# Performance work log

Hardware: AMD Instinct MI355X
Metric: run time of the kernel (lower is better)

## Reference

```python
import jax, jax.numpy as jnp
import numpy as np

SEQ_LEN, BSIZE, DIM_OBJ_QST = 128, 1024, 37
QST_DIM, HIDDEN, SLOTS = 11, 256, 20


def _linear_params(key, out_dim, in_dim):
    kw, kb = jax.random.split(key)
    # xavier_normal for weight, default uniform-ish small bias
    std = (2.0 / (in_dim + out_dim)) ** 0.5
    w = jax.random.normal(kw, (out_dim, in_dim), jnp.float32) * std
    b = jax.random.uniform(kb, (out_dim,), jnp.float32, -0.01, 0.01)
    return w, b


def setup_inputs() -> dict:
    key = jax.random.key(0)
    ks = jax.random.split(key, 10)
    memory_inputs = jax.random.normal(ks[0], (SEQ_LEN, BSIZE, DIM_OBJ_QST), jnp.float32)
    question_inputs = jax.random.normal(ks[1], (BSIZE, QST_DIM), jnp.float32)
    C_w, C_b = _linear_params(ks[2], HIDDEN, DIM_OBJ_QST)
    Q_w, Q_b = _linear_params(ks[3], HIDDEN, QST_DIM)
    H_w, H_b = _linear_params(ks[4], HIDDEN, 2 * HIDDEN)
    U_w, U_b = _linear_params(ks[5], HIDDEN, HIDDEN)
    V_w, V_b = _linear_params(ks[6], HIDDEN, HIDDEN)
    W_w, W_b = _linear_params(ks[7], HIDDEN, HIDDEN)
    J_w, J_b = _linear_params(ks[8], HIDDEN, 3 * HIDDEN)
    prelu_a = jnp.float32(1.0)  # nn.PReLU(init=1), single shared slope
    # nn.Embedding(num_mem_slots, hidden, padding_idx=0), uniform(-sqrt3, sqrt3), row 0 zeroed
    embed = jax.random.uniform(ks[9], (SLOTS, HIDDEN), jnp.float32, -(3.0 ** 0.5), 3.0 ** 0.5)
    embed = embed.at[0].set(0.0)
    return dict(memory_inputs=memory_inputs, question_inputs=question_inputs,
                C_w=C_w, C_b=C_b, Q_w=Q_w, Q_b=Q_b, H_w=H_w, H_b=H_b,
                U_w=U_w, U_b=U_b, V_w=V_w, V_b=V_b, W_w=W_w, W_b=W_b,
                J_w=J_w, J_b=J_b, prelu_a=prelu_a, embed=embed)


def reference(memory_inputs, question_inputs, C_w, C_b, Q_w, Q_b, H_w, H_b,
              U_w, U_b, V_w, V_b, W_w, W_b, J_w, J_b, prelu_a, embed):
    S, B, _ = memory_inputs.shape
    D, M = embed.shape[1], embed.shape[0]

    mi = jax.nn.relu(jnp.einsum('sbi,di->sbd', memory_inputs, C_w) + C_b)  # (S,B,D)
    q = jax.nn.relu(question_inputs @ Q_w.T + Q_b)                          # (B,D)

    # keys: embedding(arange(M)) tiled per batch, flattened to (B*M, D)
    keys = jnp.tile(embed[None, :, :], (B, 1, 1)).reshape(B * M, D)

    def step(memories, sentence):  # sentence: (B,D)
        sent = jnp.repeat(sentence, M, axis=0)                              # (B*M, D)
        gate = jax.nn.sigmoid(jnp.sum(sent * (memories + keys), axis=-1, keepdims=True))
        join = jnp.concatenate([memories @ U_w.T + U_b,
                                sent @ V_w.T + V_b,
                                keys @ W_w.T + W_b], axis=1)                # (B*M, 3D)
        j = jax.nn.relu(join) @ J_w.T + J_b
        cand = jnp.where(j > 0, j, prelu_a * j)                             # PReLU
        upd = memories + gate * cand
        upd = upd / (jnp.linalg.norm(upd, axis=-1, keepdims=True) + 1e-12)
        return upd, None

    memories, _ = jax.lax.scan(step, keys, mi)
    ng = memories.reshape(B, M, D)
    energies = jnp.sum(ng * q[:, None, :], axis=-1)                         # (B,M)
    attn = jax.nn.softmax(energies, axis=-1)
    attended = jnp.sum(ng * attn[:, :, None], axis=1)                       # (B,D)
    out = jax.nn.relu(jnp.concatenate([q, attended], axis=1) @ H_w.T + H_b)
    return out
```

## Files before the change

kernel.cpp:

```cpp
#include <hip/hip_runtime.h>
#include <hip/hip_bf16.h>


#define S_LEN 128
#define BSZ   1024
#define DOBJ  37
#define QD    11

typedef float f32x4 __attribute__((ext_vector_type(4)));
typedef short bf16x8 __attribute__((ext_vector_type(8)));
typedef short bf16x4 __attribute__((ext_vector_type(4)));

#define MFMA16(a, b, c) __builtin_amdgcn_mfma_f32_16x16x32_bf16((a), (b), (c), 0, 0, 0)

__device__ __forceinline__ float b2f(short h) {
    union { unsigned u; float f; } c; c.u = ((unsigned)(unsigned short)h) << 16; return c.f;
}
__device__ __forceinline__ short f2b(float x) {
    union { float f; unsigned u; } c; c.f = x;
    return (short)((c.u + 0x7FFFu + ((c.u >> 16) & 1u)) >> 16);
}
__device__ __forceinline__ unsigned pkbf(float a, float b) {
    union { __hip_bfloat162 h2; unsigned u; } c;
    c.h2 = __float22bfloat162_rn(make_float2(a, b));
    return c.u;
}
__device__ __forceinline__ float ld1(const void* p, int i, bool f32) {
    return f32 ? ((const float*)p)[i] : b2f(((const short*)p)[i]);
}
__device__ __forceinline__ bf16x8 ld8(const void* p, int i, bool f32) {
    if (!f32) return *(const bf16x8*)((const short*)p + i);
    const float* q = (const float*)p + i;
    bf16x8 r;
    #pragma unroll
    for (int e = 0; e < 8; ++e) r[e] = f2b(q[e]);
    return r;
}

__global__ __launch_bounds__(256, 2) void renet_phase1(
    const void* __restrict__ MI, const void* __restrict__ Cw, const void* __restrict__ Cb,
    const void* __restrict__ Vw, const void* __restrict__ Vb, const void* __restrict__ Jw,
    const void* __restrict__ PA, short* __restrict__ mi_out, short* __restrict__ jv_out)
{
    const bool F32 = (*(const unsigned*)PA == 0x3F800000u);
    __shared__ __align__(16) short A[64 * 264];
    __shared__ __align__(16) float MIL[64 * 40];
    __shared__ float VBL[256];

    const int t = threadIdx.x, r0 = blockIdx.x * 64;
    const int wv = t >> 6, lane = t & 63, lr = lane & 15, quad = lane >> 4;

    VBL[t] = ld1(Vb, t, F32);
    for (int c = 0; c < 10; ++c) {
        int idx = c * 256 + t;
        if (idx < 64 * 37) { int i = idx / 37, k = idx - i * 37; MIL[i * 40 + k] = ld1(MI, (r0 + i) * 37 + k, F32); }
    }
    __syncthreads();

    {
        float cw[DOBJ];
        #pragma unroll
        for (int k = 0; k < DOBJ; ++k) cw[k] = ld1(Cw, t * DOBJ + k, F32);
        float cb = ld1(Cb, t, F32);
        for (int i = 0; i < 64; ++i) {
            float a = cb;
            #pragma unroll
            for (int k = 0; k < DOBJ; ++k) a += MIL[i * 40 + k] * cw[k];
            short h = f2b(fmaxf(a, 0.f));
            A[i * 264 + t] = h;
            mi_out[(r0 + i) * 256 + t] = h;
        }
    }
    __syncthreads();

    const f32x4 Z4 = {0.f, 0.f, 0.f, 0.f};
    f32x4 acc[4][4];

    #pragma unroll
    for (int rt = 0; rt < 4; ++rt)
        #pragma unroll
        for (int nt = 0; nt < 4; ++nt) acc[rt][nt] = Z4;
    #pragma unroll
    for (int kt = 0; kt < 8; ++kt) {
        bf16x8 a[4];
        #pragma unroll
        for (int rt = 0; rt < 4; ++rt)
            a[rt] = *(const bf16x8*)&A[(rt * 16 + lr) * 264 + kt * 32 + quad * 8];
        #pragma unroll
        for (int nt = 0; nt < 4; ++nt) {
            int n = wv * 64 + nt * 16 + lr;
            bf16x8 b = ld8(Vw, n * 256 + kt * 32 + quad * 8, F32);
            #pragma unroll
            for (int rt = 0; rt < 4; ++rt) acc[rt][nt] = MFMA16(a[rt], b, acc[rt][nt]);
        }
    }
    __syncthreads();
    #pragma unroll
    for (int nt = 0; nt < 4; ++nt) {
        int n = wv * 64 + nt * 16 + lr;
        float vb = VBL[n];
        #pragma unroll
        for (int rt = 0; rt < 4; ++rt)
            #pragma unroll
            for (int r = 0; r < 4; ++r)
                A[(rt * 16 + quad * 4 + r) * 264 + n] = f2b(fmaxf(acc[rt][nt][r] + vb, 0.f));
    }
    __syncthreads();

    #pragma unroll
    for (int rt = 0; rt < 4; ++rt)
        #pragma unroll
        for (int nt = 0; nt < 4; ++nt) acc[rt][nt] = Z4;
    #pragma unroll
    for (int kt = 0; kt < 8; ++kt) {
        bf16x8 a[4];
        #pragma unroll
        for (int rt = 0; rt < 4; ++rt)
            a[rt] = *(const bf16x8*)&A[(rt * 16 + lr) * 264 + kt * 32 + quad * 8];
        #pragma unroll
        for (int nt = 0; nt < 4; ++nt) {
            int n = wv * 64 + nt * 16 + lr;
            bf16x8 b = ld8(Jw, n * 768 + 256 + kt * 32 + quad * 8, F32);
            #pragma unroll
            for (int rt = 0; rt < 4; ++rt) acc[rt][nt] = MFMA16(a[rt], b, acc[rt][nt]);
        }
    }
    __syncthreads();
    #pragma unroll
    for (int nt = 0; nt < 4; ++nt) {
        int n = wv * 64 + nt * 16 + lr;
        #pragma unroll
        for (int rt = 0; rt < 4; ++rt)
            #pragma unroll
            for (int r = 0; r < 4; ++r)
                A[(rt * 16 + quad * 4 + r) * 264 + n] = f2b(acc[rt][nt][r]);
    }
    __syncthreads();
    for (int c = 0; c < 16; ++c) {
        int idx = c * 1024 + t * 4;
        int i = idx >> 8, k = idx & 255;
        *(ushort4*)&jv_out[(r0 + i) * 256 + k] = *(const ushort4*)&A[i * 264 + k];
    }
}

__global__ __launch_bounds__(512, 2) void renet_recur(
    const short* __restrict__ mi, const short* __restrict__ jv,
    const void* __restrict__ Qin, const void* __restrict__ Qw, const void* __restrict__ Qb,
    const void* __restrict__ Uw, const void* __restrict__ Ub,
    const void* __restrict__ Jw, const void* __restrict__ Jb,
    const void* __restrict__ Ww, const void* __restrict__ Wb,
    const void* __restrict__ Hw, const void* __restrict__ Hb,
    const void* __restrict__ PA, const void* __restrict__ Emb, void* __restrict__ Out)
{
    const bool F32 = (*(const unsigned*)PA == 0x3F800000u);
    __shared__ __align__(16) short LDS[32208];
    short* const A1  = LDS;
    short* const STG = LDS + 15840;
    short* const SJ  = LDS + 26400;
    short* const JWL = LDS + 26928;

    const int t = threadIdx.x;
    const int w8 = t >> 6;
    const int lane = t & 63, lr = lane & 15, quad = lane >> 4;
    const int colb = w8 * 32;
    const float pa = ld1(PA, 0, F32);
    const f32x4 Z4 = {0.f, 0.f, 0.f, 0.f};
    const int bq0 = blockIdx.x * 2;

    float ub2[2][4];
    #pragma unroll
    for (int ct = 0; ct < 2; ++ct)
        #pragma unroll
        for (int r = 0; r < 4; ++r) ub2[ct][r] = ld1(Ub, colb + ct * 16 + quad * 4 + r, F32);

    bf16x8 uf[8][2], jf[8][2];
    #pragma unroll
    for (int kt = 0; kt < 8; ++kt)
        #pragma unroll
        for (int ct = 0; ct < 2; ++ct) {
            uf[kt][ct] = ld8(Uw, (colb + ct * 16 + lr) * 256 + kt * 32 + quad * 8, F32);
            jf[kt][ct] = ld8(Jw, (colb + ct * 16 + lr) * 768 + kt * 32 + quad * 8, F32);
        }

    for (int c = 0; c < 11; ++c) {
        int idx = c * 512 + t;
        if (idx < 20 * 264) {
            int row = idx / 264, k = idx - row * 264;
            A1[(40 + row) * 264 + k] = (k < 256) ? f2b(ld1(Emb, row * 256 + k, F32)) : (short)0;
        }
    }
    __syncthreads();

    {
        const int col = t & 255, grp = t >> 8, m0p = grp * 10;
        float* WKS = (float*)STG;
        float wacc[10];
        #pragma unroll
        for (int mm = 0; mm < 10; ++mm) wacc[mm] = 0.f;
        for (int c = 0; c < 32; ++c) {
            bf16x8 wv8 = ld8(Ww, col * 256 + c * 8, F32);
            float wf[8];
            #pragma unroll
            for (int e = 0; e < 8; ++e) wf[e] = b2f(wv8[e]);
            #pragma unroll
            for (int mm = 0; mm < 10; ++mm) {
                bf16x8 e8 = *(const bf16x8*)&A1[(40 + m0p + mm) * 264 + c * 8];
                float s = 0.f;
                #pragma unroll
                for (int e = 0; e < 8; ++e) s += b2f(e8[e]) * wf[e];
                wacc[mm] += s;
            }
        }
        float wb = ld1(Wb, col, F32);
        #pragma unroll
        for (int mm = 0; mm < 10; ++mm) WKS[(m0p + mm) * 256 + col] = fmaxf(wacc[mm] + wb, 0.f);
    }
    for (int c = 0; c < 21; ++c) {
        int idx = c * 512 + t;
        if (idx < 40 * 264) {
            int row = idx / 264, k = idx - row * 264;
            short v = (k < 256) ? A1[(40 + row % 20) * 264 + k] : (short)0;
            if (k == 256 || k == 257) v = (k == 257) ? (short)0x3F80 : (short)0;
            A1[idx] = v;
        }
    }
    __syncthreads();

    {
        const int col = t & 255, grp = t >> 8, m0p = grp * 10;
        const float* WKS = (const float*)STG;
        const float jb = ld1(Jb, col, F32);
        float jacc[10];
        #pragma unroll
        for (int mm = 0; mm < 10; ++mm) jacc[mm] = 0.f;
        for (int c = 0; c < 32; ++c) {
            bf16x8 j8 = ld8(Jw, col * 768 + 512 + c * 8, F32);
            float jfv[8];
            #pragma unroll
            for (int e = 0; e < 8; ++e) jfv[e] = b2f(j8[e]);
            #pragma unroll
            for (int mm = 0; mm < 10; ++mm) {
                float4 w0 = *(const float4*)&WKS[(m0p + mm) * 256 + c * 8];
                float4 w1 = *(const float4*)&WKS[(m0p + mm) * 256 + c * 8 + 4];
                jacc[mm] += w0.x * jfv[0] + w0.y * jfv[1] + w0.z * jfv[2] + w0.w * jfv[3]
                          + w1.x * jfv[4] + w1.y * jfv[5] + w1.z * jfv[6] + w1.w * jfv[7];
            }
        }
        #pragma unroll
        for (int mm = 0; mm < 10; ++mm) JWL[(m0p + mm) * 264 + col] = f2b(jacc[mm] + jb);
    }

    ushort4 pf_mi = {0, 0, 0, 0};
    if (t < 128) {
        pf_mi = *(const ushort4*)&mi[(bq0 + (t >> 6)) * 256 + (t & 63) * 4];
        *(ushort4*)&SJ[(t >> 6) * 264 + (t & 63) * 4] = pf_mi;
    }
    __syncthreads();

    for (int s = 0; s < S_LEN; ++s) {
        const int parO = (s & 1) << 1, parN = 2 - parO;

        if (s + 1 < S_LEN && t < 128)
            pf_mi = *(const ushort4*)&mi[((s + 1) * BSZ + bq0 + (t >> 6)) * 256 + (t & 63) * 4];

        float sc_o[3];
        #pragma unroll
        for (int nt = 0; nt < 3; ++nt) {
            const int row = ((nt == 0) ? 0 : (nt == 1) ? 16 : 24) + lr;
            sc_o[nt] = 1.f / (sqrtf(*(const float*)&A1[row * 264 + 256 + parO]) + 1e-12f);
        }

        if (w8 < 4) {
            const int base = (w8 == 3) ? 44 : w8 * 16;
            f32x4 ag = Z4;
            #pragma unroll
            for (int kt = 0; kt < 8; ++kt) {
                bf16x8 a = *(const bf16x8*)&SJ[lr * 264 + kt * 32 + quad * 8];
                bf16x8 b = *(const bf16x8*)&A1[(base + lr) * 264 + kt * 32 + quad * 8];
                ag = MFMA16(a, b, ag);
            }
            if (quad == 0) {
                const int row = base + lr;
                float sg = 1.f;
                if (row < 40) sg = 1.f / (sqrtf(*(const float*)&A1[row * 264 + 256 + parO]) + 1e-12f);
                float* gl = (float*)&A1[row * 264 + 260];
                gl[0] = ag[0] * sg; gl[1] = ag[1] * sg;
            }
        }

        f32x4 acc[3][2];
        #pragma unroll
        for (int nt = 0; nt < 3; ++nt) { acc[nt][0] = Z4; acc[nt][1] = Z4; }
        #pragma unroll
        for (int kt = 0; kt < 8; ++kt) {
            bf16x8 b0 = *(const bf16x8*)&A1[(0 + lr) * 264 + kt * 32 + quad * 8];
            bf16x8 b1 = *(const bf16x8*)&A1[(16 + lr) * 264 + kt * 32 + quad * 8];
            bf16x8 b2 = *(const bf16x8*)&A1[(24 + lr) * 264 + kt * 32 + quad * 8];
            acc[0][0] = MFMA16(uf[kt][0], b0, acc[0][0]);
            acc[1][0] = MFMA16(uf[kt][0], b1, acc[1][0]);
            acc[2][0] = MFMA16(uf[kt][0], b2, acc[2][0]);
            acc[0][1] = MFMA16(uf[kt][1], b0, acc[0][1]);
            acc[1][1] = MFMA16(uf[kt][1], b1, acc[1][1]);
            acc[2][1] = MFMA16(uf[kt][1], b2, acc[2][1]);
        }
        #pragma unroll
        for (int nt = 0; nt < 3; ++nt) {
            const int base = (nt == 0) ? 0 : (nt == 1) ? 16 : 24;
            #pragma unroll
            for (int ct = 0; ct < 2; ++ct) {
                uint2 pk;
                pk.x = pkbf(fmaxf(acc[nt][ct][0] * sc_o[nt] + ub2[ct][0], 0.f),
                            fmaxf(acc[nt][ct][1] * sc_o[nt] + ub2[ct][1], 0.f));
                pk.y = pkbf(fmaxf(acc[nt][ct][2] * sc_o[nt] + ub2[ct][2], 0.f),
                            fmaxf(acc[nt][ct][3] * sc_o[nt] + ub2[ct][3], 0.f));
                *(uint2*)&STG[(base + lr) * 264 + colb + ct * 16 + quad * 4] = pk;
            }
        }
        if (t < 40) *(float*)&A1[t * 264 + 256 + parN] = 0.f;
        __syncthreads();

        bf16x4 jv0[2], jv1[2];
        #pragma unroll
        for (int ct = 0; ct < 2; ++ct) {
            jv0[ct] = *(const bf16x4*)&jv[(s * BSZ + bq0) * 256 + colb + ct * 16 + quad * 4];
            jv1[ct] = *(const bf16x4*)&jv[(s * BSZ + bq0 + 1) * 256 + colb + ct * 16 + quad * 4];
        }

        f32x4 acc2[3][2];
        #pragma unroll
        for (int nt = 0; nt < 3; ++nt) { acc2[nt][0] = Z4; acc2[nt][1] = Z4; }
        #pragma unroll
        for (int kt = 0; kt < 8; ++kt) {
            bf16x8 b0 = *(const bf16x8*)&STG[(0 + lr) * 264 + kt * 32 + quad * 8];
            bf16x8 b1 = *(const bf16x8*)&STG[(16 + lr) * 264 + kt * 32 + quad * 8];
            bf16x8 b2 = *(const bf16x8*)&STG[(24 + lr) * 264 + kt * 32 + quad * 8];
            acc2[0][0] = MFMA16(jf[kt][0], b0, acc2[0][0]);
            acc2[1][0] = MFMA16(jf[kt][0], b1, acc2[1][0]);
            acc2[2][0] = MFMA16(jf[kt][0], b2, acc2[2][0]);
            acc2[0][1] = MFMA16(jf[kt][1], b0, acc2[0][1]);
            acc2[1][1] = MFMA16(jf[kt][1], b1, acc2[1][1]);
            acc2[2][1] = MFMA16(jf[kt][1], b2, acc2[2][1]);
        }

        float gate_[3];
        bf16x4 old_[3][2], jw_[3][2];
        #pragma unroll
        for (int nt = 0; nt < 3; ++nt) {
            const int base = (nt == 0) ? 0 : (nt == 1) ? 16 : 24;
            const int row = base + lr;
            const int bi = (row >= 20) ? 1 : 0;
            const int slot = row - bi * 20;
            float gp = ((const float*)&A1[row * 264 + 260])[bi]
                     + ((const float*)&A1[(40 + slot) * 264 + 260])[bi];
            gate_[nt] = 1.f / (1.f + __expf(-gp));
            jw_[nt][0]  = *(const bf16x4*)&JWL[slot * 264 + colb + quad * 4];
            jw_[nt][1]  = *(const bf16x4*)&JWL[slot * 264 + colb + 16 + quad * 4];
            old_[nt][0] = *(const bf16x4*)&A1[row * 264 + colb + quad * 4];
            old_[nt][1] = *(const bf16x4*)&A1[row * 264 + colb + 16 + quad * 4];
        }
        #pragma unroll
        for (int nt = 0; nt < 3; ++nt) {
            const int base = (nt == 0) ? 0 : (nt == 1) ? 16 : 24;
            const int row = base + lr;
            const int bi = (row >= 20) ? 1 : 0;
            float ss = 0.f;
            #pragma unroll
            for (int ct = 0; ct < 2; ++ct) {
                bf16x4 jv4 = bi ? jv1[ct] : jv0[ct];
                float u4[4];
                #pragma unroll
                for (int r = 0; r < 4; ++r) {
                    float j = acc2[nt][ct][r] + b2f(jv4[r]) + b2f(jw_[nt][ct][r]);
                    float cand = j > 0.f ? j : pa * j;
                    float u = b2f(old_[nt][ct][r]) * sc_o[nt] + gate_[nt] * cand;
                    u4[r] = u;
                    ss += u * u;
                }
                uint2 pk;
                pk.x = pkbf(u4[0], u4[1]);
                pk.y = pkbf(u4[2], u4[3]);
                *(uint2*)&A1[row * 264 + colb + ct * 16 + quad * 4] = pk;
            }
            ss += __shfl_xor(ss, 16);
            ss += __shfl_xor(ss, 32);
            if (quad == 0 && !(nt == 2 && lr < 8))
                atomicAdd((float*)&A1[row * 264 + 256 + parN], ss);
        }
        if (t < 128) *(ushort4*)&SJ[(t >> 6) * 264 + (t & 63) * 4] = pf_mi;
        __syncthreads();
    }

    float* SF = (float*)STG;
    {
        const int col = t & 255, bi = t >> 8;
        float a = ld1(Qb, col, F32);
        #pragma unroll
        for (int k = 0; k < QD; ++k)
            a += ld1(Qin, (bq0 + bi) * QD + k, F32) * ld1(Qw, col * QD + k, F32);
        SF[bi * 256 + col] = fmaxf(a, 0.f);
    }
    __syncthreads();
    if (t < 40) {
        int bi = t / 20;
        float e = 0.f;
        for (int c = 0; c < 32; ++c) {
            bf16x8 mv = *(const bf16x8*)&A1[t * 264 + c * 8];
            #pragma unroll
            for (int e8 = 0; e8 < 8; ++e8) e += b2f(mv[e8]) * SF[bi * 256 + c * 8 + e8];
        }
        float scf = 1.f / (sqrtf(*(const float*)&A1[t * 264 + 256]) + 1e-12f);
        SF[1536 + t] = e * scf;
    }
    __syncthreads();
    if (t < 2) {
        float mx = -1e30f;
        for (int m = 0; m < 20; ++m) mx = fmaxf(mx, SF[1536 + t * 20 + m]);
        float sm = 0.f, ex[20];
        for (int m = 0; m < 20; ++m) { ex[m] = __expf(SF[1536 + t * 20 + m] - mx); sm += ex[m]; }
        float inv = 1.f / sm;
        for (int m = 0; m < 20; ++m) {
            float scf = 1.f / (sqrtf(*(const float*)&A1[(t * 20 + m) * 264 + 256]) + 1e-12f);
            SF[1576 + t * 20 + m] = ex[m] * inv * scf;
        }
    }
    __syncthreads();
    {
        const int col = t & 255, bi = t >> 8;
        float a = 0.f;
        for (int m = 0; m < 20; ++m)
            a += SF[1576 + bi * 20 + m] * b2f(A1[(bi * 20 + m) * 264 + col]);
        SF[512 + bi * 512 + 256 + col] = a;
        SF[512 + bi * 512 + col] = SF[bi * 256 + col];
    }
    __syncthreads();
    {
        const int col = t & 255, bi = t >> 8;
        float o = ld1(Hb, col, F32);
        for (int c = 0; c < 64; ++c) {
            bf16x8 hv = ld8(Hw, col * 512 + c * 8, F32);
            #pragma unroll
            for (int e8 = 0; e8 < 8; ++e8) o += b2f(hv[e8]) * SF[512 + bi * 512 + c * 8 + e8];
        }
        int oi = (bq0 + bi) * 256 + col;
        float v = fmaxf(o, 0.f);
        if (F32) ((float*)Out)[oi] = v; else ((short*)Out)[oi] = f2b(v);
    }
}

extern "C" void kernel_launch(void* const* d_in, const int* in_sizes, int n_in,
                              void* d_out, int out_size, void* d_ws, size_t ws_size,
                              hipStream_t stream) {
    (void)in_sizes; (void)n_in; (void)out_size; (void)ws_size;
    const void* MIp = d_in[0];
    const void* Qin = d_in[1];
    const void* Cw  = d_in[2];
    const void* Cb  = d_in[3];
    const void* Qw  = d_in[4];
    const void* Qb  = d_in[5];
    const void* Hw  = d_in[6];
    const void* Hb  = d_in[7];
    const void* Uw  = d_in[8];
    const void* Ub  = d_in[9];
    const void* Vw  = d_in[10];
    const void* Vb  = d_in[11];
    const void* Ww  = d_in[12];
    const void* Wb  = d_in[13];
    const void* Jw  = d_in[14];
    const void* Jb  = d_in[15];
    const void* PA  = d_in[16];
    const void* Emb = d_in[17];

    short* mi_ws = (short*)d_ws;
    short* jv_ws = mi_ws + (size_t)S_LEN * BSZ * 256;

    renet_phase1<<<dim3(2048), dim3(256), 0, stream>>>(MIp, Cw, Cb, Vw, Vb, Jw, PA, mi_ws, jv_ws);
    renet_recur<<<dim3(512), dim3(512), 0, stream>>>(mi_ws, jv_ws, Qin, Qw, Qb, Uw, Ub,
                                                     Jw, Jb, Ww, Wb, Hw, Hb, PA, Emb, d_out);
}
```

Before: 1.527 ms.

## Process four batch elements per block in recurrent kernel instead of two

The recurrent kernel now handles 4 batch items (80 memory rows) per workgroup instead of 2 (40 rows, padded to 48). The MFMA tiles grow from 3 to 5 row tiles, so the register-resident U and J weight fragments are reused across more rows and the padding waste drops. The gate computation is extended to 4 batch columns, and the grid halves to 256 blocks. In exchange, LDS use rises to about 105KB per block and there are fewer blocks than the GPU has CUs, so occupancy and parallelism fall.

```diff
diff --git a/kernel.cpp b/kernel.cpp
--- a/kernel.cpp
+++ b/kernel.cpp
@@ -153,11 +153,11 @@
     const void* __restrict__ PA, const void* __restrict__ Emb, void* __restrict__ Out)
 {
     const bool F32 = (*(const unsigned*)PA == 0x3F800000u);
-    __shared__ __align__(16) short LDS[32208];
+    __shared__ __align__(16) short LDS[53856];
     short* const A1  = LDS;
-    short* const STG = LDS + 15840;
-    short* const SJ  = LDS + 26400;
-    short* const JWL = LDS + 26928;
+    short* const STG = LDS + 26400;
+    short* const SJ  = LDS + 47520;
+    short* const JWL = LDS + 48576;
 
     const int t = threadIdx.x;
     const int w8 = t >> 6;
@@ -165,7 +165,7 @@
     const int colb = w8 * 32;
     const float pa = ld1(PA, 0, F32);
     const f32x4 Z4 = {0.f, 0.f, 0.f, 0.f};
-    const int bq0 = blockIdx.x * 2;
+    const int bq0 = blockIdx.x * 4;
 
     float ub2[2][4];
     #pragma unroll
@@ -186,7 +186,7 @@
         int idx = c * 512 + t;
         if (idx < 20 * 264) {
             int row = idx / 264, k = idx - row * 264;
-            A1[(40 + row) * 264 + k] = (k < 256) ? f2b(ld1(Emb, row * 256 + k, F32)) : (short)0;
+            A1[(80 + row) * 264 + k] = (k < 256) ? f2b(ld1(Emb, row * 256 + k, F32)) : (short)0;
         }
     }
     __syncthreads();
@@ -204,7 +204,7 @@
             for (int e = 0; e < 8; ++e) wf[e] = b2f(wv8[e]);
             #pragma unroll
             for (int mm = 0; mm < 10; ++mm) {
-                bf16x8 e8 = *(const bf16x8*)&A1[(40 + m0p + mm) * 264 + c * 8];
+                bf16x8 e8 = *(const bf16x8*)&A1[(80 + m0p + mm) * 264 + c * 8];
                 float s = 0.f;
                 #pragma unroll
                 for (int e = 0; e < 8; ++e) s += b2f(e8[e]) * wf[e];
@@ -215,11 +215,11 @@
         #pragma unroll
         for (int mm = 0; mm < 10; ++mm) WKS[(m0p + mm) * 256 + col] = fmaxf(wacc[mm] + wb, 0.f);
     }
-    for (int c = 0; c < 21; ++c) {
+    for (int c = 0; c < 42; ++c) {
         int idx = c * 512 + t;
-        if (idx < 40 * 264) {
+        if (idx < 80 * 264) {
             int row = idx / 264, k = idx - row * 264;
-            short v = (k < 256) ? A1[(40 + row % 20) * 264 + k] : (short)0;
+            short v = (k < 256) ? A1[(80 + row % 20) * 264 + k] : (short)0;
             if (k == 256 || k == 257) v = (k == 257) ? (short)0x3F80 : (short)0;
             A1[idx] = v;
         }
@@ -251,7 +251,7 @@
     }
 
     ushort4 pf_mi = {0, 0, 0, 0};
-    if (t < 128) {
+    if (t < 256) {
         pf_mi = *(const ushort4*)&mi[(bq0 + (t >> 6)) * 256 + (t & 63) * 4];
         *(ushort4*)&SJ[(t >> 6) * 264 + (t & 63) * 4] = pf_mi;
     }
@@ -260,18 +260,16 @@
     for (int s = 0; s < S_LEN; ++s) {
         const int parO = (s & 1) << 1, parN = 2 - parO;
 
-        if (s + 1 < S_LEN && t < 128)
+        if (s + 1 < S_LEN && t < 256)
             pf_mi = *(const ushort4*)&mi[((s + 1) * BSZ + bq0 + (t >> 6)) * 256 + (t & 63) * 4];
 
-        float sc_o[3];
-        #pragma unroll
-        for (int nt = 0; nt < 3; ++nt) {
-            const int row = ((nt == 0) ? 0 : (nt == 1) ? 16 : 24) + lr;
-            sc_o[nt] = 1.f / (sqrtf(*(const float*)&A1[row * 264 + 256 + parO]) + 1e-12f);
-        }
-
-        if (w8 < 4) {
-            const int base = (w8 == 3) ? 44 : w8 * 16;
+        float sc_o[5];
+        #pragma unroll
+        for (int nt = 0; nt < 5; ++nt)
+            sc_o[nt] = 1.f / (sqrtf(*(const float*)&A1[(nt * 16 + lr) * 264 + 256 + parO]) + 1e-12f);
+
+        if (w8 < 7) {
+            const int base = (w8 < 5) ? w8 * 16 : (w8 == 5) ? 80 : 84;
             f32x4 ag = Z4;
             #pragma unroll
             for (int kt = 0; kt < 8; ++kt) {
@@ -281,31 +279,41 @@
             }
             if (quad == 0) {
                 const int row = base + lr;
-                float sg = 1.f;
-                if (row < 40) sg = 1.f / (sqrtf(*(const float*)&A1[row * 264 + 256 + parO]) + 1e-12f);
-                float* gl = (float*)&A1[row * 264 + 260];
-                gl[0] = ag[0] * sg; gl[1] = ag[1] * sg;
-            }
-        }
-
-        f32x4 acc[3][2];
-        #pragma unroll
-        for (int nt = 0; nt < 3; ++nt) { acc[nt][0] = Z4; acc[nt][1] = Z4; }
+                if (row < 80) {
+                    const int bi = row / 20;
+                    float sg = 1.f / (sqrtf(*(const float*)&A1[row * 264 + 256 + parO]) + 1e-12f);
+                    float gm = (bi == 0) ? ag[0] : (bi == 1) ? ag[1] : (bi == 2) ? ag[2] : ag[3];
+                    *(float*)&A1[row * 264 + 260] = gm * sg;
+                } else {
+                    float* gl = (float*)&A1[row * 264 + 256];
+                    gl[0] = ag[0]; gl[1] = ag[1]; gl[2] = ag[2]; gl[3] = ag[3];
+                }
+            }
+        }
+
+        f32x4 acc[5][2];
+        #pragma unroll
+        for (int nt = 0; nt < 5; ++nt) { acc[nt][0] = Z4; acc[nt][1] = Z4; }
         #pragma unroll
         for (int kt = 0; kt < 8; ++kt) {
-            bf16x8 b0 = *(const bf16x8*)&A1[(0 + lr) * 264 + kt * 32 + quad * 8];
+            bf16x8 b0 = *(const bf16x8*)&A1[( 0 + lr) * 264 + kt * 32 + quad * 8];
             bf16x8 b1 = *(const bf16x8*)&A1[(16 + lr) * 264 + kt * 32 + quad * 8];
-            bf16x8 b2 = *(const bf16x8*)&A1[(24 + lr) * 264 + kt * 32 + quad * 8];
+            bf16x8 b2 = *(const bf16x8*)&A1[(32 + lr) * 264 + kt * 32 + quad * 8];
+            bf16x8 b3 = *(const bf16x8*)&A1[(48 + lr) * 264 + kt * 32 + quad * 8];
+            bf16x8 b4 = *(const bf16x8*)&A1[(64 + lr) * 264 + kt * 32 + quad * 8];
             acc[0][0] = MFMA16(uf[kt][0], b0, acc[0][0]);
             acc[1][0] = MFMA16(uf[kt][0], b1, acc[1][0]);
             acc[2][0] = MFMA16(uf[kt][0], b2, acc[2][0]);
+            acc[3][0] = MFMA16(uf[kt][0], b3, acc[3][0]);
+            acc[4][0] = MFMA16(uf[kt][0], b4, acc[4][0]);
             acc[0][1] = MFMA16(uf[kt][1], b0, acc[0][1]);
             acc[1][1] = MFMA16(uf[kt][1], b1, acc[1][1]);
             acc[2][1] = MFMA16(uf[kt][1], b2, acc[2][1]);
-        }
-        #pragma unroll
-        for (int nt = 0; nt < 3; ++nt) {
-            const int base = (nt == 0) ? 0 : (nt == 1) ? 16 : 24;
+            acc[3][1] = MFMA16(uf[kt][1], b3, acc[3][1]);
+            acc[4][1] = MFMA16(uf[kt][1], b4, acc[4][1]);
+        }
+        #pragma unroll
+        for (int nt = 0; nt < 5; ++nt) {
             #pragma unroll
             for (int ct = 0; ct < 2; ++ct) {
                 uint2 pk;
@@ -313,66 +321,64 @@
                             fmaxf(acc[nt][ct][1] * sc_o[nt] + ub2[ct][1], 0.f));
                 pk.y = pkbf(fmaxf(acc[nt][ct][2] * sc_o[nt] + ub2[ct][2], 0.f),
                             fmaxf(acc[nt][ct][3] * sc_o[nt] + ub2[ct][3], 0.f));
-                *(uint2*)&STG[(base + lr) * 264 + colb + ct * 16 + quad * 4] = pk;
-            }
-        }
-        if (t < 40) *(float*)&A1[t * 264 + 256 + parN] = 0.f;
+                *(uint2*)&STG[(nt * 16 + lr) * 264 + colb + ct * 16 + quad * 4] = pk;
+            }
+        }
+        if (t < 80) *(float*)&A1[t * 264 + 256 + parN] = 0.f;
         __syncthreads();
 
-        bf16x4 jv0[2], jv1[2];
+        bf16x4 jvb0[2], jvb1[2], jvb2[2], jvb3[2];
         #pragma unroll
         for (int ct = 0; ct < 2; ++ct) {
-            jv0[ct] = *(const bf16x4*)&jv[(s * BSZ + bq0) * 256 + colb + ct * 16 + quad * 4];
-            jv1[ct] = *(const bf16x4*)&jv[(s * BSZ + bq0 + 1) * 256 + colb + ct * 16 + quad * 4];
-        }
-
-        f32x4 acc2[3][2];
-        #pragma unroll
-        for (int nt = 0; nt < 3; ++nt) { acc2[nt][0] = Z4; acc2[nt][1] = Z4; }
+            const int co = colb + ct * 16 + quad * 4;
+            jvb0[ct] = *(const bf16x4*)&jv[(s * BSZ + bq0 + 0) * 256 + co];
+            jvb1[ct] = *(const bf16x4*)&jv[(s * BSZ + bq0 + 1) * 256 + co];
+            jvb2[ct] = *(const bf16x4*)&jv[(s * BSZ + bq0 + 2) * 256 + co];
+            jvb3[ct] = *(const bf16x4*)&jv[(s * BSZ + bq0 + 3) * 256 + co];
+        }
+
+        f32x4 acc2[5][2];
+        #pragma unroll
+        for (int nt = 0; nt < 5; ++nt) { acc2[nt][0] = Z4; acc2[nt][1] = Z4; }
         #pragma unroll
         for (int kt = 0; kt < 8; ++kt) {
-            bf16x8 b0 = *(const bf16x8*)&STG[(0 + lr) * 264 + kt * 32 + quad * 8];
+            bf16x8 b0 = *(const bf16x8*)&STG[( 0 + lr) * 264 + kt * 32 + quad * 8];
             bf16x8 b1 = *(const bf16x8*)&STG[(16 + lr) * 264 + kt * 32 + quad * 8];
-            bf16x8 b2 = *(const bf16x8*)&STG[(24 + lr) * 264 + kt * 32 + quad * 8];
+            bf16x8 b2 = *(const bf16x8*)&STG[(32 + lr) * 264 + kt * 32 + quad * 8];
+            bf16x8 b3 = *(const bf16x8*)&STG[(48 + lr) * 264 + kt * 32 + quad * 8];
+            bf16x8 b4 = *(const bf16x8*)&STG[(64 + lr) * 264 + kt * 32 + quad * 8];
             acc2[0][0] = MFMA16(jf[kt][0], b0, acc2[0][0]);
             acc2[1][0] = MFMA16(jf[kt][0], b1, acc2[1][0]);
             acc2[2][0] = MFMA16(jf[kt][0], b2, acc2[2][0]);
+            acc2[3][0] = MFMA16(jf[kt][0], b3, acc2[3][0]);
+            acc2[4][0] = MFMA16(jf[kt][0], b4, acc2[4][0]);
             acc2[0][1] = MFMA16(jf[kt][1], b0, acc2[0][1]);
             acc2[1][1] = MFMA16(jf[kt][1], b1, acc2[1][1]);
             acc2[2][1] = MFMA16(jf[kt][1], b2, acc2[2][1]);
-        }
-
-        float gate_[3];
-        bf16x4 old_[3][2], jw_[3][2];
-        #pragma unroll
-        for (int nt = 0; nt < 3; ++nt) {
-            const int base = (nt == 0) ? 0 : (nt == 1) ? 16 : 24;
-            const int row = base + lr;
-            const int bi = (row >= 20) ? 1 : 0;
+            acc2[3][1] = MFMA16(jf[kt][1], b3, acc2[3][1]);
+            acc2[4][1] = MFMA16(jf[kt][1], b4, acc2[4][1]);
+        }
+
+        #pragma unroll
+        for (int nt = 0; nt < 5; ++nt) {
+            const int row = nt * 16 + lr;
+            const int bi = row / 20;
             const int slot = row - bi * 20;
-            float gp = ((const float*)&A1[row * 264 + 260])[bi]
-                     + ((const float*)&A1[(40 + slot) * 264 + 260])[bi];
-            gate_[nt] = 1.f / (1.f + __expf(-gp));
-            jw_[nt][0]  = *(const bf16x4*)&JWL[slot * 264 + colb + quad * 4];
-            jw_[nt][1]  = *(const bf16x4*)&JWL[slot * 264 + colb + 16 + quad * 4];
-            old_[nt][0] = *(const bf16x4*)&A1[row * 264 + colb + quad * 4];
-            old_[nt][1] = *(const bf16x4*)&A1[row * 264 + colb + 16 + quad * 4];
-        }
-        #pragma unroll
-        for (int nt = 0; nt < 3; ++nt) {
-            const int base = (nt == 0) ? 0 : (nt == 1) ? 16 : 24;
-            const int row = base + lr;
-            const int bi = (row >= 20) ? 1 : 0;
+            float gp = *(const float*)&A1[row * 264 + 260]
+                     + ((const float*)&A1[(80 + slot) * 264 + 256])[bi];
+            float gate = 1.f / (1.f + __expf(-gp));
             float ss = 0.f;
             #pragma unroll
             for (int ct = 0; ct < 2; ++ct) {
-                bf16x4 jv4 = bi ? jv1[ct] : jv0[ct];
+                bf16x4 jw4  = *(const bf16x4*)&JWL[slot * 264 + colb + ct * 16 + quad * 4];
+                bf16x4 old4 = *(const bf16x4*)&A1[row * 264 + colb + ct * 16 + quad * 4];
+                bf16x4 jv4  = (bi == 0) ? jvb0[ct] : (bi == 1) ? jvb1[ct] : (bi == 2) ? jvb2[ct] : jvb3[ct];
                 float u4[4];
                 #pragma unroll
                 for (int r = 0; r < 4; ++r) {
-                    float j = acc2[nt][ct][r] + b2f(jv4[r]) + b2f(jw_[nt][ct][r]);
+                    float j = acc2[nt][ct][r] + b2f(jv4[r]) + b2f(jw4[r]);
                     float cand = j > 0.f ? j : pa * j;
-                    float u = b2f(old_[nt][ct][r]) * sc_o[nt] + gate_[nt] * cand;
+                    float u = b2f(old4[r]) * sc_o[nt] + gate * cand;
                     u4[r] = u;
                     ss += u * u;
                 }
@@ -383,16 +389,17 @@
             }
             ss += __shfl_xor(ss, 16);
             ss += __shfl_xor(ss, 32);
-            if (quad == 0 && !(nt == 2 && lr < 8))
+            if (quad == 0)
                 atomicAdd((float*)&A1[row * 264 + 256 + parN], ss);
         }
-        if (t < 128) *(ushort4*)&SJ[(t >> 6) * 264 + (t & 63) * 4] = pf_mi;
+        if (t < 256) *(ushort4*)&SJ[(t >> 6) * 264 + (t & 63) * 4] = pf_mi;
         __syncthreads();
     }
 
     float* SF = (float*)STG;
-    {
-        const int col = t & 255, bi = t >> 8;
+    #pragma unroll
+    for (int it = 0; it < 2; ++it) {
+        const int idx = it * 512 + t, col = idx & 255, bi = idx >> 8;
         float a = ld1(Qb, col, F32);
         #pragma unroll
         for (int k = 0; k < QD; ++k)
@@ -400,7 +407,7 @@
         SF[bi * 256 + col] = fmaxf(a, 0.f);
     }
     __syncthreads();
-    if (t < 40) {
+    if (t < 80) {
         int bi = t / 20;
         float e = 0.f;
         for (int c = 0; c < 32; ++c) {
@@ -409,37 +416,39 @@
             for (int e8 = 0; e8 < 8; ++e8) e += b2f(mv[e8]) * SF[bi * 256 + c * 8 + e8];
         }
         float scf = 1.f / (sqrtf(*(const float*)&A1[t * 264 + 256]) + 1e-12f);
-        SF[1536 + t] = e * scf;
-    }
-    __syncthreads();
-    if (t < 2) {
+        SF[1024 + t] = e * scf;
+    }
+    __syncthreads();
+    if (t < 4) {
         float mx = -1e30f;
-        for (int m = 0; m < 20; ++m) mx = fmaxf(mx, SF[1536 + t * 20 + m]);
+        for (int m = 0; m < 20; ++m) mx = fmaxf(mx, SF[1024 + t * 20 + m]);
         float sm = 0.f, ex[20];
-        for (int m = 0; m < 20; ++m) { ex[m] = __expf(SF[1536 + t * 20 + m] - mx); sm += ex[m]; }
+        for (int m = 0; m < 20; ++m) { ex[m] = __expf(SF[1024 + t * 20 + m] - mx); sm += ex[m]; }
         float inv = 1.f / sm;
         for (int m = 0; m < 20; ++m) {
             float scf = 1.f / (sqrtf(*(const float*)&A1[(t * 20 + m) * 264 + 256]) + 1e-12f);
-            SF[1576 + t * 20 + m] = ex[m] * inv * scf;
-        }
-    }
-    __syncthreads();
-    {
-        const int col = t & 255, bi = t >> 8;
+            SF[1104 + t * 20 + m] = ex[m] * inv * scf;
+        }
+    }
+    __syncthreads();
+    #pragma unroll
+    for (int it = 0; it < 2; ++it) {
+        const int idx = it * 512 + t, col = idx & 255, bi = idx >> 8;
         float a = 0.f;
         for (int m = 0; m < 20; ++m)
-            a += SF[1576 + bi * 20 + m] * b2f(A1[(bi * 20 + m) * 264 + col]);
-        SF[512 + bi * 512 + 256 + col] = a;
-        SF[512 + bi * 512 + col] = SF[bi * 256 + col];
-    }
-    __syncthreads();
-    {
-        const int col = t & 255, bi = t >> 8;
+            a += SF[1104 + bi * 20 + m] * b2f(A1[(bi * 20 + m) * 264 + col]);
+        SF[1280 + bi * 512 + 256 + col] = a;
+        SF[1280 + bi * 512 + col] = SF[bi * 256 + col];
+    }
+    __syncthreads();
+    #pragma unroll
+    for (int it = 0; it < 2; ++it) {
+        const int idx = it * 512 + t, col = idx & 255, bi = idx >> 8;
         float o = ld1(Hb, col, F32);
         for (int c = 0; c < 64; ++c) {
             bf16x8 hv = ld8(Hw, col * 512 + c * 8, F32);
             #pragma unroll
-            for (int e8 = 0; e8 < 8; ++e8) o += b2f(hv[e8]) * SF[512 + bi * 512 + c * 8 + e8];
+            for (int e8 = 0; e8 < 8; ++e8) o += b2f(hv[e8]) * SF[1280 + bi * 512 + c * 8 + e8];
         }
         int oi = (bq0 + bi) * 256 + col;
         float v = fmaxf(o, 0.f);
@@ -474,6 +483,6 @@
     short* jv_ws = mi_ws + (size_t)S_LEN * BSZ * 256;
 
     renet_phase1<<<dim3(2048), dim3(256), 0, stream>>>(MIp, Cw, Cb, Vw, Vb, Jw, PA, mi_ws, jv_ws);
-    renet_recur<<<dim3(512), dim3(512), 0, stream>>>(mi_ws, jv_ws, Qin, Qw, Qb, Uw, Ub,
+    renet_recur<<<dim3(256), dim3(512), 0, stream>>>(mi_ws, jv_ws, Qin, Qw, Qb, Uw, Ub,
                                                      Jw, Jb, Ww, Wb, Hw, Hb, PA, Emb, d_out);
 }
```

Result: faster. 1.351 ms (-11.6%).
